# Kernel tuning notes

Hardware: AMD Instinct MI355X
Metric: run time of the kernel (lower is better)

The kernel has to match this reference:

```python
import jax, jax.numpy as jnp
import numpy as np

DIM = 2048
HEADS = 16
KV_HEADS = 4
DIM_HEAD = 128
INNER = HEADS * DIM_HEAD          # 2048
KV_INNER = KV_HEADS * DIM_HEAD    # 512
FF = 4 * DIM                      # 8192
QK_SCALE = 10.0                   # x-transformers default qk_norm_scale
B, S = 2, 2048


def layer_norm(x, g, b, eps=1e-5):
    m = jnp.mean(x, axis=-1, keepdims=True)
    v = jnp.mean((x - m) ** 2, axis=-1, keepdims=True)
    return (x - m) * jax.lax.rsqrt(v + eps) * g + b


def l2norm(t, eps=1e-12):
    n = jnp.sqrt(jnp.sum(t * t, axis=-1, keepdims=True))
    return t / jnp.maximum(n, eps)


def setup_inputs() -> dict:
    key = jax.random.key(0)
    ks = jax.random.split(key, 12)
    s = lambda fan_in: 1.0 / np.sqrt(fan_in)
    return {
        "x":     jax.random.normal(ks[0], (B, S, DIM), jnp.float32),
        "wq":    jax.random.normal(ks[1], (DIM, INNER), jnp.float32) * s(DIM),
        "wk":    jax.random.normal(ks[2], (DIM, KV_INNER), jnp.float32) * s(DIM),
        "wv":    jax.random.normal(ks[3], (DIM, KV_INNER), jnp.float32) * s(DIM),
        "wo":    jax.random.normal(ks[4], (INNER, DIM), jnp.float32) * s(INNER),
        "ln1_g": jnp.ones((DIM,), jnp.float32),
        "ln1_b": jnp.zeros((DIM,), jnp.float32),
        "w1":    jax.random.normal(ks[5], (DIM, FF), jnp.float32) * s(DIM),
        "b1":    jnp.zeros((FF,), jnp.float32),
        "lnf_g": jnp.ones((FF,), jnp.float32),
        "lnf_b": jnp.zeros((FF,), jnp.float32),
        "w2":    jax.random.normal(ks[6], (FF, DIM), jnp.float32) * s(FF),
        "b2":    jnp.zeros((DIM,), jnp.float32),
    }


def reference(x, wq, wk, wv, wo, ln1_g, ln1_b, w1, b1, lnf_g, lnf_b, w2, b2):
    b, s, _ = x.shape
    rep = HEADS // KV_HEADS
    # GQA projections
    q = (x @ wq).reshape(b, s, HEADS, DIM_HEAD).transpose(0, 2, 1, 3)      # [b,h,s,d]
    k = (x @ wk).reshape(b, s, KV_HEADS, DIM_HEAD).transpose(0, 2, 1, 3)   # [b,g,s,d]
    v = (x @ wv).reshape(b, s, KV_HEADS, DIM_HEAD).transpose(0, 2, 1, 3)
    # qk-norm: l2-normalize q/k along head dim, fixed scale
    q = l2norm(q)
    k = l2norm(k)
    k = jnp.repeat(k, rep, axis=1)  # expand kv heads to query heads
    v = jnp.repeat(v, rep, axis=1)
    scores = jnp.einsum("bhid,bhjd->bhij", q, k) * QK_SCALE
    attn = jax.nn.softmax(scores, axis=-1)
    o = jnp.einsum("bhij,bhjd->bhid", attn, v)
    o = o.transpose(0, 2, 1, 3).reshape(b, s, INNER) @ wo
    # post-attention LayerNorm (no residual in the source)
    h = layer_norm(o, ln1_g, ln1_b)
    # FFN: SiLU + post-activation LayerNorm (dropout inert in eval)
    f = jax.nn.silu(h @ w1 + b1)
    f = layer_norm(f, lnf_g, lnf_b)
    y = f @ w2 + b2
    # the source re-applies the SAME norm after the ffn
    return layer_norm(y, ln1_g, ln1_b)
```

## Files before the change

### kernel.cpp

```cpp
#include <hip/hip_runtime.h>


typedef __attribute__((ext_vector_type(8))) short short8;
typedef __attribute__((ext_vector_type(4))) float f32x4;

__device__ __forceinline__ unsigned short f2bf(float f) {
  unsigned int u = __builtin_bit_cast(unsigned int, f);
  u += 0x7FFFu + ((u >> 16) & 1u);
  return (unsigned short)(u >> 16);
}
__device__ __forceinline__ float bf2f(unsigned short h) {
  unsigned int u = ((unsigned int)h) << 16;
  return __builtin_bit_cast(float, u);
}

typedef const void __attribute__((address_space(1)))* gas1_t;
typedef void __attribute__((address_space(3)))* las3_t;
#define GLDS16(g, l) \
  __builtin_amdgcn_global_load_lds((gas1_t)(const void*)(g), (las3_t)(void*)(l), 16, 0, 0)

__global__ __launch_bounds__(256) void cast_f32_bf16(const float* __restrict__ src,
                                                     unsigned short* __restrict__ dst,
                                                     int n) {
  int i = (blockIdx.x * 256 + threadIdx.x) * 4;
  if (i >= n) return;
  float4 f = *(const float4*)(src + i);
  uint2 u;
  u.x = (unsigned)f2bf(f.x) | ((unsigned)f2bf(f.y) << 16);
  u.y = (unsigned)f2bf(f.z) | ((unsigned)f2bf(f.w) << 16);
  *(uint2*)(dst + i) = u;
}

__global__ void transcast(const float* __restrict__ src, unsigned short* __restrict__ dst,
                          int R, int C, int dst_ld, int row_off) {
  __shared__ float t[32][33];
  const int tx = threadIdx.x, ty = threadIdx.y;
  const int c0 = blockIdx.x * 32, r0 = blockIdx.y * 32;
#pragma unroll
  for (int j = 0; j < 4; ++j)
    t[ty + j * 8][tx] = src[(size_t)(r0 + ty + j * 8) * C + c0 + tx];
  __syncthreads();
#pragma unroll
  for (int j = 0; j < 4; ++j)
    dst[(size_t)(row_off + c0 + ty + j * 8) * dst_ld + r0 + tx] = f2bf(t[tx][ty + j * 8]);
}

template <int BN>
__global__ __launch_bounds__(512, 2) void gemm256(const unsigned short* __restrict__ A,
                                                  const unsigned short* __restrict__ Bt,
                                                  unsigned short* __restrict__ C,
                                                  int M, int N, int K) {
  constexpr int NF = BN / 64;
  constexpr int HB = BN * 64;
  constexpr int RB = BN / 128;
  constexpr int AK1 = 16384 + HB;
  constexpr int BUFB = 32768 + 2 * HB;
  extern __shared__ char lds[];

  const int tid = threadIdx.x, l = tid & 63, w = tid >> 6;
  const int wr = w >> 2, wc = w & 3;
  const int brow = blockIdx.y * 256, bcol = blockIdx.x * BN;
  const unsigned short* Aa = A + (size_t)brow * K;
  const unsigned short* Bb = Bt + (size_t)bcol * K;
  const int NT = K >> 6;

  const int slot = l >> 4;
  const int rowA = wr * 128 + (l & 15);
  const int aRd = ((((rowA << 2) | slot) << 4) ^ ((rowA & 7) << 4));
  const int rowB = wc * (BN / 4) + (l & 15);
  const int bRd = ((((rowB << 2) | slot) << 4) ^ ((rowB & 7) << 4));

  f32x4 acc[8][NF];
#pragma unroll
  for (int m = 0; m < 8; ++m)
#pragma unroll
    for (int n = 0; n < NF; ++n) acc[m][n] = (f32x4){0.f, 0.f, 0.f, 0.f};

  auto stageA = [&](char* dst, int kofs) {
#pragma unroll
    for (int r = 0; r < 2; ++r) {
      const int g = r * 512 + tid;
      const int rw = ((g >> 3) << 1) | (((g >> 2) ^ (g >> 4)) & 1);
      const int sl = (g ^ rw) & 3;
      GLDS16(Aa + (size_t)rw * K + kofs + sl * 8, dst + g * 16);
    }
  };
  auto stageB = [&](char* dst, int kofs) {
#pragma unroll
    for (int r = 0; r < RB; ++r) {
      const int g = r * 512 + tid;
      const int rw = ((g >> 3) << 1) | (((g >> 2) ^ (g >> 4)) & 1);
      const int sl = (g ^ rw) & 3;
      GLDS16(Bb + (size_t)rw * K + kofs + sl * 8, dst + g * 16);
    }
  };

  stageA(lds, 0);
  stageB(lds + 16384, 0);
  stageA(lds + AK1, 32);
  stageB(lds + AK1 + 16384, 32);

  int kt = 0;
  for (int t = 0; t < NT; ++t) {
    char* curb = lds + (t & 1) * BUFB;
    char* nxtb = lds + ((t & 1) ^ 1) * BUFB;
    const int ktn = (t + 1 < NT) ? kt + 64 : 0;
    short8 af[4], bf[NF];

    if constexpr (BN == 256) asm volatile("s_waitcnt vmcnt(4)" ::: "memory");
    else                     asm volatile("s_waitcnt vmcnt(3)" ::: "memory");
    asm volatile("s_barrier" ::: "memory");
#pragma unroll
    for (int n = 0; n < NF; ++n) bf[n] = *(const short8*)(curb + 16384 + bRd + n * 1024);
#pragma unroll
    for (int m = 0; m < 4; ++m) af[m] = *(const short8*)(curb + aRd + m * 1024);
    stageA(nxtb, ktn);
    __builtin_amdgcn_s_setprio(1);
#pragma unroll
    for (int m = 0; m < 4; ++m)
#pragma unroll
      for (int n = 0; n < NF; ++n)
        acc[m][n] = __builtin_amdgcn_mfma_f32_16x16x32_bf16(af[m], bf[n], acc[m][n], 0, 0, 0);
    __builtin_amdgcn_s_setprio(0);

    asm volatile("s_barrier" ::: "memory");
#pragma unroll
    for (int m = 0; m < 4; ++m) af[m] = *(const short8*)(curb + aRd + (m + 4) * 1024);
    stageB(nxtb + 16384, ktn);
    __builtin_amdgcn_s_setprio(1);
#pragma unroll
    for (int m = 0; m < 4; ++m)
#pragma unroll
      for (int n = 0; n < NF; ++n)
        acc[m + 4][n] = __builtin_amdgcn_mfma_f32_16x16x32_bf16(af[m], bf[n], acc[m + 4][n], 0, 0, 0);
    __builtin_amdgcn_s_setprio(0);

    if constexpr (BN == 256) asm volatile("s_waitcnt vmcnt(4)" ::: "memory");
    else                     asm volatile("s_waitcnt vmcnt(3)" ::: "memory");
    asm volatile("s_barrier" ::: "memory");
#pragma unroll
    for (int n = 0; n < NF; ++n) bf[n] = *(const short8*)(curb + AK1 + 16384 + bRd + n * 1024);
#pragma unroll
    for (int m = 0; m < 4; ++m) af[m] = *(const short8*)(curb + AK1 + aRd + m * 1024);
    stageA(nxtb + AK1, ktn + 32);
    __builtin_amdgcn_s_setprio(1);
#pragma unroll
    for (int m = 0; m < 4; ++m)
#pragma unroll
      for (int n = 0; n < NF; ++n)
        acc[m][n] = __builtin_amdgcn_mfma_f32_16x16x32_bf16(af[m], bf[n], acc[m][n], 0, 0, 0);
    __builtin_amdgcn_s_setprio(0);

    asm volatile("s_barrier" ::: "memory");
#pragma unroll
    for (int m = 0; m < 4; ++m) af[m] = *(const short8*)(curb + AK1 + aRd + (m + 4) * 1024);
    stageB(nxtb + AK1 + 16384, ktn + 32);
    __builtin_amdgcn_s_setprio(1);
#pragma unroll
    for (int m = 0; m < 4; ++m)
#pragma unroll
      for (int n = 0; n < NF; ++n)
        acc[m + 4][n] = __builtin_amdgcn_mfma_f32_16x16x32_bf16(af[m], bf[n], acc[m + 4][n], 0, 0, 0);
    __builtin_amdgcn_s_setprio(0);

    kt += 64;
  }

#pragma unroll
  for (int m = 0; m < 8; ++m)
#pragma unroll
    for (int r = 0; r < 4; ++r) {
      const int row = brow + wr * 128 + m * 16 + (l >> 4) * 4 + r;
#pragma unroll
      for (int n = 0; n < NF; ++n) {
        const int col = bcol + wc * (BN / 4) + n * 16 + (l & 15);
        C[(size_t)row * N + col] = f2bf(acc[m][n][r]);
      }
    }
}

__global__ __launch_bounds__(256) void l2norm_qk(unsigned short* __restrict__ qkv) {
  const int wid = blockIdx.x * 4 + (threadIdx.x >> 6);
  const int l = threadIdx.x & 63;
  const int token = wid / 20, u = wid % 20;
  const int col = (u < 16) ? u * 128 : 2048 + (u - 16) * 128;
  unsigned short* p = qkv + (size_t)token * 3072 + col + l * 2;
  const float a = bf2f(p[0]), b = bf2f(p[1]);
  float ss = a * a + b * b;
#pragma unroll
  for (int m = 1; m < 64; m <<= 1) ss += __shfl_xor(ss, m);
  const float sc = ((u < 16) ? 10.f : 1.f) / fmaxf(sqrtf(ss), 1e-12f);
  p[0] = f2bf(a * sc);
  p[1] = f2bf(b * sc);
}

__global__ __launch_bounds__(256) void vtrans(const unsigned short* __restrict__ qkv,
                                              unsigned short* __restrict__ vt) {
  const int idx = blockIdx.x * 256 + threadIdx.x;
  const int s_ = idx & 2047;
  const int rest = idx >> 11;
  const int d = rest & 127;
  const int bg = rest >> 7;
  const int b = bg >> 2, g = bg & 3;
  vt[idx] = qkv[(size_t)(b * 2048 + s_) * 3072 + 2560 + g * 128 + d];
}

__global__ __launch_bounds__(256) void attn_kernel(const unsigned short* __restrict__ qkv,
                                                   const unsigned short* __restrict__ vt,
                                                   unsigned short* __restrict__ out) {
  __shared__ unsigned short Kl[64 * 136];
  __shared__ unsigned short Vl[128 * 72];
  __shared__ unsigned short Pl[4 * 16 * 72];
  const int tid = threadIdx.x, w = tid >> 6, l = tid & 63;
  const int bh = blockIdx.y, b = bh >> 4, h = bh & 15, g = h >> 2;
  const int q0 = blockIdx.x * 64;

  short8 qf[4];
  {
    const unsigned short* qrow =
        qkv + (size_t)(b * 2048 + q0 + w * 16 + (l & 15)) * 3072 + h * 128;
#pragma unroll
    for (int kk = 0; kk < 4; ++kk)
      qf[kk] = *(const short8*)&qrow[kk * 32 + (l >> 4) * 8];
  }

  f32x4 o[8];
#pragma unroll
  for (int n = 0; n < 8; ++n) o[n] = (f32x4){0.f, 0.f, 0.f, 0.f};
  float m_r[4] = {-1e30f, -1e30f, -1e30f, -1e30f};
  float l_r[4] = {0.f, 0.f, 0.f, 0.f};

  const unsigned short* kbase = qkv + (size_t)(b * 2048) * 3072 + 2048 + g * 128;
  const unsigned short* vbase = vt + (size_t)(b * 4 + g) * 128 * 2048;

  for (int t = 0; t < 32; ++t) {
    const int kv0 = t * 64;
    __syncthreads();
#pragma unroll
    for (int i = 0; i < 4; ++i) {
      const int row = i * 16 + (tid >> 4), ce = (tid & 15) * 8;
      *(uint4*)&Kl[row * 136 + ce] = *(const uint4*)&kbase[(size_t)(kv0 + row) * 3072 + ce];
    }
#pragma unroll
    for (int i = 0; i < 4; ++i) {
      const int d = i * 32 + (tid >> 3), ce = (tid & 7) * 8;
      *(uint4*)&Vl[d * 72 + ce] = *(const uint4*)&vbase[(size_t)d * 2048 + kv0 + ce];
    }
    __syncthreads();

    f32x4 s[4];
#pragma unroll
    for (int c = 0; c < 4; ++c) s[c] = (f32x4){0.f, 0.f, 0.f, 0.f};
#pragma unroll
    for (int kk = 0; kk < 4; ++kk)
#pragma unroll
      for (int c = 0; c < 4; ++c) {
        short8 kf = *(const short8*)&Kl[(c * 16 + (l & 15)) * 136 + kk * 32 + (l >> 4) * 8];
        s[c] = __builtin_amdgcn_mfma_f32_16x16x32_bf16(qf[kk], kf, s[c], 0, 0, 0);
      }

    float alpha[4];
#pragma unroll
    for (int r = 0; r < 4; ++r) {
      float tm = fmaxf(fmaxf(s[0][r], s[1][r]), fmaxf(s[2][r], s[3][r]));
#pragma unroll
      for (int mm = 1; mm < 16; mm <<= 1) tm = fmaxf(tm, __shfl_xor(tm, mm));
      const float mn = fmaxf(m_r[r], tm);
      float ps = 0.f;
#pragma unroll
      for (int c = 0; c < 4; ++c) {
        const float p = __expf(s[c][r] - mn);
        s[c][r] = p;
        ps += p;
      }
#pragma unroll
      for (int mm = 1; mm < 16; mm <<= 1) ps += __shfl_xor(ps, mm);
      alpha[r] = __expf(m_r[r] - mn);
      l_r[r] = l_r[r] * alpha[r] + ps;
      m_r[r] = mn;
    }
#pragma unroll
    for (int n = 0; n < 8; ++n)
#pragma unroll
      for (int r = 0; r < 4; ++r) o[n][r] *= alpha[r];

#pragma unroll
    for (int c = 0; c < 4; ++c)
#pragma unroll
      for (int r = 0; r < 4; ++r)
        Pl[w * 1152 + ((l >> 4) * 4 + r) * 72 + c * 16 + (l & 15)] = f2bf(s[c][r]);
    __syncthreads();

#pragma unroll
    for (int kk = 0; kk < 2; ++kk) {
      short8 pf = *(const short8*)&Pl[w * 1152 + (l & 15) * 72 + kk * 32 + (l >> 4) * 8];
#pragma unroll
      for (int n = 0; n < 8; ++n) {
        short8 vf = *(const short8*)&Vl[(n * 16 + (l & 15)) * 72 + kk * 32 + (l >> 4) * 8];
        o[n] = __builtin_amdgcn_mfma_f32_16x16x32_bf16(pf, vf, o[n], 0, 0, 0);
      }
    }
  }

  unsigned short* orow = out + (size_t)(b * 2048 + q0 + w * 16) * 2048 + h * 128;
#pragma unroll
  for (int r = 0; r < 4; ++r) {
    const float inv = 1.f / l_r[r];
    const int row = (l >> 4) * 4 + r;
#pragma unroll
    for (int n = 0; n < 8; ++n)
      orow[(size_t)row * 2048 + n * 16 + (l & 15)] = f2bf(o[n][r] * inv);
  }
}

template <int NC, bool BIAS, bool SILU, bool OUTF32>
__global__ __launch_bounds__(256) void ln_row(const unsigned short* __restrict__ src,
                                              unsigned short* __restrict__ dstb,
                                              float* __restrict__ dstf,
                                              const float* __restrict__ gamma,
                                              const float* __restrict__ beta,
                                              const float* __restrict__ bias) {
  constexpr int E = NC / 256;
  const int row = blockIdx.x, tid = threadIdx.x;
  const size_t base = (size_t)row * NC + tid * E;
  float v[E];
#pragma unroll
  for (int c = 0; c < E / 8; ++c) {
    uint4 u = *(const uint4*)(src + base + c * 8);
    const unsigned short* us = (const unsigned short*)&u;
#pragma unroll
    for (int j = 0; j < 8; ++j) v[c * 8 + j] = bf2f(us[j]);
  }
  if constexpr (BIAS) {
#pragma unroll
    for (int i = 0; i < E; ++i) v[i] += bias[tid * E + i];
  }
  if constexpr (SILU) {
#pragma unroll
    for (int i = 0; i < E; ++i) v[i] = v[i] / (1.f + __expf(-v[i]));
  }
  float s = 0.f, q = 0.f;
#pragma unroll
  for (int i = 0; i < E; ++i) {
    s += v[i];
    q += v[i] * v[i];
  }
#pragma unroll
  for (int m = 1; m < 64; m <<= 1) {
    s += __shfl_xor(s, m);
    q += __shfl_xor(q, m);
  }
  __shared__ float rs[4], rq[4];
  if ((tid & 63) == 0) {
    rs[tid >> 6] = s;
    rq[tid >> 6] = q;
  }
  __syncthreads();
  s = rs[0] + rs[1] + rs[2] + rs[3];
  q = rq[0] + rq[1] + rq[2] + rq[3];
  const float mean = s / NC;
  const float rstd = rsqrtf(q / NC - mean * mean + 1e-5f);
#pragma unroll
  for (int i = 0; i < E; ++i)
    v[i] = (v[i] - mean) * rstd * gamma[tid * E + i] + beta[tid * E + i];
  if constexpr (OUTF32) {
#pragma unroll
    for (int c = 0; c < E / 4; ++c) {
      float4 f = {v[c * 4], v[c * 4 + 1], v[c * 4 + 2], v[c * 4 + 3]};
      *(float4*)(dstf + base + c * 4) = f;
    }
  } else {
#pragma unroll
    for (int c = 0; c < E / 8; ++c) {
      uint4 u;
      unsigned* up = (unsigned*)&u;
#pragma unroll
      for (int j = 0; j < 4; ++j)
        up[j] = (unsigned)f2bf(v[c * 8 + j * 2]) | ((unsigned)f2bf(v[c * 8 + j * 2 + 1]) << 16);
      *(uint4*)(dstb + base + c * 8) = u;
    }
  }
}

extern "C" void kernel_launch(void* const* d_in, const int* in_sizes, int n_in,
                              void* d_out, int out_size, void* d_ws, size_t ws_size,
                              hipStream_t stream) {
  (void)in_sizes; (void)n_in; (void)out_size; (void)ws_size;
  const float* x     = (const float*)d_in[0];
  const float* wq    = (const float*)d_in[1];
  const float* wk    = (const float*)d_in[2];
  const float* wv    = (const float*)d_in[3];
  const float* wo    = (const float*)d_in[4];
  const float* ln1_g = (const float*)d_in[5];
  const float* ln1_b = (const float*)d_in[6];
  const float* w1    = (const float*)d_in[7];
  const float* b1    = (const float*)d_in[8];
  const float* lnf_g = (const float*)d_in[9];
  const float* lnf_b = (const float*)d_in[10];
  const float* w2    = (const float*)d_in[11];
  const float* b2    = (const float*)d_in[12];

  unsigned short* ws = (unsigned short*)d_ws;
  unsigned short* wqkvT  = ws;
  unsigned short* woT    = wqkvT  + (size_t)3072 * 2048;
  unsigned short* w1T    = woT    + (size_t)2048 * 2048;
  unsigned short* w2T    = w1T    + (size_t)8192 * 2048;
  unsigned short* xb     = w2T    + (size_t)2048 * 8192;
  unsigned short* qkv    = xb     + (size_t)4096 * 2048;
  unsigned short* vt     = qkv    + (size_t)4096 * 3072;
  unsigned short* attn_o = vt     + (size_t)4096 * 512;
  unsigned short* f1     = attn_o + (size_t)4096 * 2048;

  (void)hipFuncSetAttribute((const void*)gemm256<256>,
                            hipFuncAttributeMaxDynamicSharedMemorySize, 131072);
  (void)hipFuncSetAttribute((const void*)gemm256<128>,
                            hipFuncAttributeMaxDynamicSharedMemorySize, 98304);

  const dim3 tb(32, 8);
  cast_f32_bf16<<<8192, 256, 0, stream>>>(x, xb, 4096 * 2048);
  transcast<<<dim3(64, 64),  tb, 0, stream>>>(wq, wqkvT, 2048, 2048, 2048, 0);
  transcast<<<dim3(16, 64),  tb, 0, stream>>>(wk, wqkvT, 2048, 512, 2048, 2048);
  transcast<<<dim3(16, 64),  tb, 0, stream>>>(wv, wqkvT, 2048, 512, 2048, 2560);
  transcast<<<dim3(64, 64),  tb, 0, stream>>>(wo, woT, 2048, 2048, 2048, 0);
  transcast<<<dim3(256, 64), tb, 0, stream>>>(w1, w1T, 2048, 8192, 2048, 0);
  transcast<<<dim3(64, 256), tb, 0, stream>>>(w2, w2T, 8192, 2048, 8192, 0);

  gemm256<256><<<dim3(12, 16), 512, 131072, stream>>>(xb, wqkvT, qkv, 4096, 3072, 2048);
  l2norm_qk<<<20480, 256, 0, stream>>>(qkv);
  vtrans<<<8192, 256, 0, stream>>>(qkv, vt);
  attn_kernel<<<dim3(32, 32), 256, 0, stream>>>(qkv, vt, attn_o);
  gemm256<128><<<dim3(16, 16), 512, 98304, stream>>>(attn_o, woT, xb, 4096, 2048, 2048);
  ln_row<2048, false, false, false><<<4096, 256, 0, stream>>>(xb, xb, nullptr, ln1_g, ln1_b, nullptr);
  gemm256<256><<<dim3(32, 16), 512, 131072, stream>>>(xb, w1T, f1, 4096, 8192, 2048);
  ln_row<8192, true, true, false><<<4096, 256, 0, stream>>>(f1, f1, nullptr, lnf_g, lnf_b, b1);
  gemm256<128><<<dim3(16, 16), 512, 98304, stream>>>(f1, w2T, qkv, 4096, 2048, 8192);
  ln_row<2048, true, false, true><<<4096, 256, 0, stream>>>(qkv, nullptr, (float*)d_out, ln1_g, ln1_b, b2);
}
```

Before: 748.8 us.

## Rewrite attention with 32x32 MFMA, fixed softmax max, double-buffered swizzled K/V

Rewrites the attention kernel to use 32x32x16 bf16 MFMA with 256-query tiles per 512-thread block. K/V tiles are prefetched into registers and double-buffered in XOR-swizzled LDS. Because q and k are l2-normalized and scaled by 10, the softmax subtracts a constant bound of 10 instead of tracking a running max. This drops the per-tile max reductions, rescaling of the output, and the LDS round-trip for P, which is now rearranged in registers via lane shuffles. The grid shrinks to 256 blocks, which risks low occupancy, and P rounding changes slightly.

```diff
diff --git a/kernel.cpp b/kernel.cpp
--- a/kernel.cpp
+++ b/kernel.cpp
@@ -3,6 +3,7 @@
 
 typedef __attribute__((ext_vector_type(8))) short short8;
 typedef __attribute__((ext_vector_type(4))) float f32x4;
+typedef __attribute__((ext_vector_type(16))) float f32x16;
 
 __device__ __forceinline__ unsigned short f2bf(float f) {
   unsigned int u = __builtin_bit_cast(unsigned int, f);
@@ -205,111 +206,152 @@
   vt[idx] = qkv[(size_t)(b * 2048 + s_) * 3072 + 2560 + g * 128 + d];
 }
 
-__global__ __launch_bounds__(256) void attn_kernel(const unsigned short* __restrict__ qkv,
+__global__ __launch_bounds__(512) void attn_kernel(const unsigned short* __restrict__ qkv,
                                                    const unsigned short* __restrict__ vt,
                                                    unsigned short* __restrict__ out) {
-  __shared__ unsigned short Kl[64 * 136];
-  __shared__ unsigned short Vl[128 * 72];
-  __shared__ unsigned short Pl[4 * 16 * 72];
+  extern __shared__ char smem[];
   const int tid = threadIdx.x, w = tid >> 6, l = tid & 63;
-  const int bh = blockIdx.y, b = bh >> 4, h = bh & 15, g = h >> 2;
-  const int q0 = blockIdx.x * 64;
-
-  short8 qf[4];
-  {
-    const unsigned short* qrow =
-        qkv + (size_t)(b * 2048 + q0 + w * 16 + (l & 15)) * 3072 + h * 128;
-#pragma unroll
-    for (int kk = 0; kk < 4; ++kk)
-      qf[kk] = *(const short8*)&qrow[kk * 32 + (l >> 4) * 8];
-  }
-
-  f32x4 o[8];
-#pragma unroll
-  for (int n = 0; n < 8; ++n) o[n] = (f32x4){0.f, 0.f, 0.f, 0.f};
-  float m_r[4] = {-1e30f, -1e30f, -1e30f, -1e30f};
-  float l_r[4] = {0.f, 0.f, 0.f, 0.f};
+  const int hi = l >> 5, l31 = l & 31;
+
+  const int n = blockIdx.x;
+  const int np = (n & 7) * 32 + (n >> 3);
+  const int qi = np & 7, bh = np >> 3;
+  const int b = bh >> 4, h = bh & 15, g = h >> 2;
+  const int q0 = qi * 256;
 
   const unsigned short* kbase = qkv + (size_t)(b * 2048) * 3072 + 2048 + g * 128;
   const unsigned short* vbase = vt + (size_t)(b * 4 + g) * 128 * 2048;
 
+  short8 qf[8];
+  {
+    const unsigned short* qrow = qkv + (size_t)(b * 2048 + q0 + w * 32 + l31) * 3072 + h * 128;
+#pragma unroll
+    for (int st = 0; st < 8; ++st)
+      qf[st] = *(const short8*)&qrow[st * 16 + hi * 8];
+  }
+
+  f32x16 o[4];
+#pragma unroll
+  for (int d0 = 0; d0 < 4; ++d0)
+#pragma unroll
+    for (int i = 0; i < 16; ++i) o[d0][i] = 0.f;
+  float l_part = 0.f;
+
+  const int krow = tid >> 3, kc = (tid & 7) * 2;
+  const int vd = tid >> 2, vc = (tid & 3) * 2;
+  const unsigned short* kg = kbase + (size_t)krow * 3072 + kc * 8;
+  const unsigned short* vg = vbase + (size_t)vd * 2048 + vc * 8;
+  const int ko0 = krow * 256 + ((kc ^ (krow & 15)) << 4);
+  const int ko1 = krow * 256 + (((kc + 1) ^ (krow & 15)) << 4);
+  const int vrp = vd >> 1, vcl = (vd & 1) * 8;
+  const int vo0 = vrp * 256 + (((vcl + vc) ^ (vrp & 15)) << 4);
+  const int vo1 = vrp * 256 + (((vcl + vc + 1) ^ (vrp & 15)) << 4);
+
+  {
+    uint4 k0 = *(const uint4*)kg, k1 = *(const uint4*)(kg + 8);
+    uint4 v0 = *(const uint4*)vg, v1 = *(const uint4*)(vg + 8);
+    char* Kb = smem;
+    char* Vb = smem + 16384;
+    *(uint4*)(Kb + ko0) = k0; *(uint4*)(Kb + ko1) = k1;
+    *(uint4*)(Vb + vo0) = v0; *(uint4*)(Vb + vo1) = v1;
+  }
+  __syncthreads();
+
+  const int swzk = l31 & 15;
   for (int t = 0; t < 32; ++t) {
-    const int kv0 = t * 64;
+    uint4 k0, k1, v0, v1;
+    const bool more = (t + 1) < 32;
+    if (more) {
+      const size_t kvo = (size_t)(t + 1) * 64;
+      k0 = *(const uint4*)(kg + kvo * 3072);
+      k1 = *(const uint4*)(kg + kvo * 3072 + 8);
+      v0 = *(const uint4*)(vg + kvo);
+      v1 = *(const uint4*)(vg + kvo + 8);
+    }
+
+    char* Kb = smem + (t & 1) * 32768;
+    char* Vb = Kb + 16384;
+
+    f32x16 s0, s1;
+#pragma unroll
+    for (int i = 0; i < 16; ++i) { s0[i] = 0.f; s1[i] = 0.f; }
+    __builtin_amdgcn_s_setprio(1);
+#pragma unroll
+    for (int st = 0; st < 8; ++st) {
+      const int ch = st * 2 + hi;
+      short8 kf0 = *(const short8*)(Kb + l31 * 256 + ((ch ^ swzk) << 4));
+      short8 kf1 = *(const short8*)(Kb + (l31 + 32) * 256 + ((ch ^ swzk) << 4));
+      s0 = __builtin_amdgcn_mfma_f32_32x32x16_bf16(kf0, qf[st], s0, 0, 0, 0);
+      s1 = __builtin_amdgcn_mfma_f32_32x32x16_bf16(kf1, qf[st], s1, 0, 0, 0);
+    }
+    __builtin_amdgcn_s_setprio(0);
+
+#pragma unroll
+    for (int i = 0; i < 16; ++i) {
+      s0[i] = __expf(s0[i] - 10.f);
+      s1[i] = __expf(s1[i] - 10.f);
+      l_part += s0[i] + s1[i];
+    }
+
+    short8 pa[4];
+#pragma unroll
+    for (int ks = 0; ks < 4; ++ks) {
+      const f32x16& sv = (ks < 2) ? s0 : s1;
+      const int base = (ks & 1) * 8;
+      auto pk = [](float x, float y) -> unsigned {
+        unsigned ux = __builtin_bit_cast(unsigned, x);
+        unsigned uy = __builtin_bit_cast(unsigned, y);
+        return ((uy + 0x8000u) & 0xFFFF0000u) | ((ux + 0x8000u) >> 16);
+      };
+      unsigned a = pk(sv[base + 0], sv[base + 1]);
+      unsigned bq = pk(sv[base + 4], sv[base + 5]);
+      unsigned c = pk(sv[base + 2], sv[base + 3]);
+      unsigned d = pk(sv[base + 6], sv[base + 7]);
+      unsigned as = __shfl_xor(a, 32), bs = __shfl_xor(bq, 32);
+      unsigned cs = __shfl_xor(c, 32), ds = __shfl_xor(d, 32);
+      uint4 wv;
+      wv.x = (l < 32) ? a : bs;
+      wv.y = (l < 32) ? c : ds;
+      wv.z = (l < 32) ? as : bq;
+      wv.w = (l < 32) ? cs : d;
+      pa[ks] = __builtin_bit_cast(short8, wv);
+    }
+
+    __builtin_amdgcn_s_setprio(1);
+#pragma unroll
+    for (int ks = 0; ks < 4; ++ks) {
+#pragma unroll
+      for (int d0 = 0; d0 < 4; ++d0) {
+        const int dd = d0 * 32 + l31;
+        const int rp = dd >> 1;
+        const int cl = ((dd & 1) * 8 + ks * 2 + hi) ^ (rp & 15);
+        short8 vf = *(const short8*)(Vb + rp * 256 + (cl << 4));
+        o[d0] = __builtin_amdgcn_mfma_f32_32x32x16_bf16(pa[ks], vf, o[d0], 0, 0, 0);
+      }
+    }
+    __builtin_amdgcn_s_setprio(0);
+
     __syncthreads();
-#pragma unroll
-    for (int i = 0; i < 4; ++i) {
-      const int row = i * 16 + (tid >> 4), ce = (tid & 15) * 8;
-      *(uint4*)&Kl[row * 136 + ce] = *(const uint4*)&kbase[(size_t)(kv0 + row) * 3072 + ce];
-    }
-#pragma unroll
-    for (int i = 0; i < 4; ++i) {
-      const int d = i * 32 + (tid >> 3), ce = (tid & 7) * 8;
-      *(uint4*)&Vl[d * 72 + ce] = *(const uint4*)&vbase[(size_t)d * 2048 + kv0 + ce];
+    if (more) {
+      char* Kn = smem + ((t + 1) & 1) * 32768;
+      char* Vn = Kn + 16384;
+      *(uint4*)(Kn + ko0) = k0; *(uint4*)(Kn + ko1) = k1;
+      *(uint4*)(Vn + vo0) = v0; *(uint4*)(Vn + vo1) = v1;
     }
     __syncthreads();
-
-    f32x4 s[4];
-#pragma unroll
-    for (int c = 0; c < 4; ++c) s[c] = (f32x4){0.f, 0.f, 0.f, 0.f};
-#pragma unroll
-    for (int kk = 0; kk < 4; ++kk)
-#pragma unroll
-      for (int c = 0; c < 4; ++c) {
-        short8 kf = *(const short8*)&Kl[(c * 16 + (l & 15)) * 136 + kk * 32 + (l >> 4) * 8];
-        s[c] = __builtin_amdgcn_mfma_f32_16x16x32_bf16(qf[kk], kf, s[c], 0, 0, 0);
-      }
-
-    float alpha[4];
-#pragma unroll
-    for (int r = 0; r < 4; ++r) {
-      float tm = fmaxf(fmaxf(s[0][r], s[1][r]), fmaxf(s[2][r], s[3][r]));
-#pragma unroll
-      for (int mm = 1; mm < 16; mm <<= 1) tm = fmaxf(tm, __shfl_xor(tm, mm));
-      const float mn = fmaxf(m_r[r], tm);
-      float ps = 0.f;
-#pragma unroll
-      for (int c = 0; c < 4; ++c) {
-        const float p = __expf(s[c][r] - mn);
-        s[c][r] = p;
-        ps += p;
-      }
-#pragma unroll
-      for (int mm = 1; mm < 16; mm <<= 1) ps += __shfl_xor(ps, mm);
-      alpha[r] = __expf(m_r[r] - mn);
-      l_r[r] = l_r[r] * alpha[r] + ps;
-      m_r[r] = mn;
-    }
-#pragma unroll
-    for (int n = 0; n < 8; ++n)
-#pragma unroll
-      for (int r = 0; r < 4; ++r) o[n][r] *= alpha[r];
-
-#pragma unroll
-    for (int c = 0; c < 4; ++c)
-#pragma unroll
-      for (int r = 0; r < 4; ++r)
-        Pl[w * 1152 + ((l >> 4) * 4 + r) * 72 + c * 16 + (l & 15)] = f2bf(s[c][r]);
-    __syncthreads();
-
-#pragma unroll
-    for (int kk = 0; kk < 2; ++kk) {
-      short8 pf = *(const short8*)&Pl[w * 1152 + (l & 15) * 72 + kk * 32 + (l >> 4) * 8];
-#pragma unroll
-      for (int n = 0; n < 8; ++n) {
-        short8 vf = *(const short8*)&Vl[(n * 16 + (l & 15)) * 72 + kk * 32 + (l >> 4) * 8];
-        o[n] = __builtin_amdgcn_mfma_f32_16x16x32_bf16(pf, vf, o[n], 0, 0, 0);
-      }
-    }
-  }
-
-  unsigned short* orow = out + (size_t)(b * 2048 + q0 + w * 16) * 2048 + h * 128;
-#pragma unroll
-  for (int r = 0; r < 4; ++r) {
-    const float inv = 1.f / l_r[r];
-    const int row = (l >> 4) * 4 + r;
-#pragma unroll
-    for (int n = 0; n < 8; ++n)
-      orow[(size_t)row * 2048 + n * 16 + (l & 15)] = f2bf(o[n][r] * inv);
+  }
+
+  float ltot = l_part + __shfl_xor(l_part, 32);
+  float linv = 1.f / ltot;
+  const int tok_base = b * 2048 + q0 + w * 32;
+#pragma unroll
+  for (int r = 0; r < 16; ++r) {
+    const int qr = (r & 3) + 8 * (r >> 2) + 4 * hi;
+    const float li = __shfl(linv, qr);
+    unsigned short* orow = out + (size_t)(tok_base + qr) * 2048 + h * 128 + l31;
+#pragma unroll
+    for (int d0 = 0; d0 < 4; ++d0)
+      orow[d0 * 32] = f2bf(o[d0][r] * li);
   }
 }
 
@@ -415,6 +457,8 @@
                             hipFuncAttributeMaxDynamicSharedMemorySize, 131072);
   (void)hipFuncSetAttribute((const void*)gemm256<128>,
                             hipFuncAttributeMaxDynamicSharedMemorySize, 98304);
+  (void)hipFuncSetAttribute((const void*)attn_kernel,
+                            hipFuncAttributeMaxDynamicSharedMemorySize, 65536);
 
   const dim3 tb(32, 8);
   cast_f32_bf16<<<8192, 256, 0, stream>>>(x, xb, 4096 * 2048);
@@ -428,7 +472,7 @@
   gemm256<256><<<dim3(12, 16), 512, 131072, stream>>>(xb, wqkvT, qkv, 4096, 3072, 2048);
   l2norm_qk<<<20480, 256, 0, stream>>>(qkv);
   vtrans<<<8192, 256, 0, stream>>>(qkv, vt);
-  attn_kernel<<<dim3(32, 32), 256, 0, stream>>>(qkv, vt, attn_o);
+  attn_kernel<<<256, 512, 65536, stream>>>(qkv, vt, attn_o);
   gemm256<128><<<dim3(16, 16), 512, 98304, stream>>>(attn_o, woT, xb, 4096, 2048, 2048);
   ln_row<2048, false, false, false><<<4096, 256, 0, stream>>>(xb, xb, nullptr, ln1_g, ln1_b, nullptr);
   gemm256<256><<<dim3(32, 16), 512, 131072, stream>>>(xb, w1T, f1, 4096, 8192, 2048);
```

Measured after the change: 651.3 us. 13.0% less time.
